# Optimization experiments

Hardware: AMD Instinct MI355X
Metric: run time of the kernel (lower is better)

## Reference

```python
import jax, jax.numpy as jnp
import numpy as np

D_MODEL, EMB_DIM, MLP_ORDER, SEQ_LEN, BATCH = 768, 3, 16, 8192, 8


def setup_inputs() -> dict:
    key = jax.random.key(0)
    ks = jax.random.split(key, 12)
    L = SEQ_LEN
    # PositionalEmbedding buffers (deterministic, as in __init__)
    t = jnp.linspace(0.0, 1.0, L)[None, :, None]                      # [1, L, 1]
    bands = (EMB_DIM - 1) // 2                                        # = 1
    t_long = jnp.linspace(0.0, L - 1.0, L)[None, :, None]
    w = 2.0 * jnp.pi * t_long / L
    f = jnp.linspace(1e-4, bands - 1.0, bands)[None, None]
    zc = jnp.exp(-1j * f * w)
    z = jnp.concatenate([t, zc.real, zc.imag], axis=-1).astype(jnp.float32)  # [1, L, 3]
    # ExponentialModulation deltas (deterministic)
    max_decay = jnp.log(0.01) / 0.3
    min_decay = jnp.log(0.01) / 1.5
    deltas = jnp.linspace(min_decay, max_decay, D_MODEL)[None, None].astype(jnp.float32)  # [1,1,D]
    s = 0.1
    return {
        "x": jax.random.normal(ks[0], (BATCH, D_MODEL, L), jnp.float32),
        "L": L,
        "z": z,
        "t": t.astype(jnp.float32),
        "deltas": deltas,
        "freq": jnp.ones((1, MLP_ORDER), jnp.float32),
        "W0": jax.random.normal(ks[1], (EMB_DIM, MLP_ORDER), jnp.float32) * s,
        "b0": jax.random.normal(ks[2], (MLP_ORDER,), jnp.float32) * s,
        "W1": jax.random.normal(ks[3], (MLP_ORDER, MLP_ORDER), jnp.float32) * s,
        "b1": jax.random.normal(ks[4], (MLP_ORDER,), jnp.float32) * s,
        "W2": jax.random.normal(ks[5], (MLP_ORDER, MLP_ORDER), jnp.float32) * s,
        "b2": jax.random.normal(ks[6], (MLP_ORDER,), jnp.float32) * s,
        "W3": jax.random.normal(ks[7], (MLP_ORDER, D_MODEL), jnp.float32) * s,
        "b3": jax.random.normal(ks[8], (D_MODEL,), jnp.float32) * s,
        "bias": jax.random.normal(ks[9], (D_MODEL,), jnp.float32),
    }


def reference(x, L, z, t, deltas, freq, W0, b0, W1, b1, W2, b2, W3, b3, bias):
    # filter generation: MLP with shared Sin activation, then exponential modulation
    zl = z[:, :L]
    h = jnp.sin(freq * (zl @ W0 + b0))
    h = jnp.sin(freq * (h @ W1 + b1))
    h = jnp.sin(freq * (h @ W2 + b2))
    h = h @ W3 + b3                               # [1, L, D]
    h = h * jnp.exp(-t[:, :L] * jnp.abs(deltas))  # exponential modulation
    k = h[0].T                                    # [D, L]
    # fftconv: causal long convolution via zero-padded FFT + skip x*bias
    fft_size = 2 * L
    y = jnp.fft.irfft(jnp.fft.rfft(x, n=fft_size) * jnp.fft.rfft(k, n=fft_size), n=fft_size)[..., :L]
    return y + x * bias[:, None]
```

## Files before the change

kernel.cpp:

```cpp
#include <hip/hip_runtime.h>
#include <math.h>


#define LSEQ 8192
#define NCH 768
#define NBATCH 8
#define NT 512

#define OFF_TWB  0
#define OFF_TW16 1024
#define OFF_TL   5124
#define OFF_TWC  6660
#define OFF_H    10240
#define OFF_KF   141312

__device__ __forceinline__ float2 cadd(float2 a, float2 b){ return make_float2(a.x+b.x, a.y+b.y); }
__device__ __forceinline__ float2 csub(float2 a, float2 b){ return make_float2(a.x-b.x, a.y-b.y); }
__device__ __forceinline__ float2 cmul(float2 a, float2 b){ return make_float2(a.x*b.x - a.y*b.y, a.x*b.y + a.y*b.x); }
__device__ __forceinline__ float2 mni(float2 a){ return make_float2(a.y, -a.x); }

__device__ __forceinline__ void wave_sync(){
    asm volatile("s_waitcnt lgkmcnt(0)" ::: "memory");
}

__device__ __forceinline__ int IDX(int i){ return i ^ (((i>>4) ^ (i>>8)) & 15); }
__device__ __forceinline__ int drev(int k){
    return ((k & 15) << 9) | (((k >> 4) & 15) << 5) | (((k >> 8) & 15) << 1) | (k >> 12);
}

#define C1 0.923879532511286756f
#define S1 0.382683432365089772f
#define R2 0.707106781186547524f

template<bool FULL>
__device__ __forceinline__ void dft16(float2 q[16]) {
    if constexpr (FULL) {
#pragma unroll
        for (int j = 0; j < 8; ++j) { float2 u=q[j], v=q[j+8]; q[j]=cadd(u,v); q[j+8]=csub(u,v); }
    }
    q[9]  = cmul(q[9],  make_float2( C1,-S1));
    q[10] = cmul(q[10], make_float2( R2,-R2));
    q[11] = cmul(q[11], make_float2( S1,-C1));
    q[12] = mni(q[12]);
    q[13] = cmul(q[13], make_float2(-S1,-C1));
    q[14] = cmul(q[14], make_float2(-R2,-R2));
    q[15] = cmul(q[15], make_float2(-C1,-S1));
#pragma unroll
    for (int b = 0; b < 16; b += 8) {
#pragma unroll
        for (int j = 0; j < 4; ++j) { float2 u=q[b+j], v=q[b+j+4]; q[b+j]=cadd(u,v); q[b+j+4]=csub(u,v); }
        q[b+5] = cmul(q[b+5], make_float2( R2,-R2));
        q[b+6] = mni(q[b+6]);
        q[b+7] = cmul(q[b+7], make_float2(-R2,-R2));
    }
#pragma unroll
    for (int b = 0; b < 16; b += 4) {
        float2 u0=q[b], v0=q[b+2], u1=q[b+1], v1=q[b+3];
        q[b]=cadd(u0,v0); q[b+2]=csub(u0,v0);
        q[b+1]=cadd(u1,v1); q[b+3]=mni(csub(u1,v1));
    }
#pragma unroll
    for (int b = 0; b < 16; b += 2) { float2 u=q[b], v=q[b+1]; q[b]=cadd(u,v); q[b+1]=csub(u,v); }
}

template<int PASS>
__device__ __forceinline__ int psb(int t) {
    if constexpr (PASS == 0) {
        return t ^ (((t>>4) ^ (t>>8)) & 15);
    } else if constexpr (PASS == 1) {
        int p = t & 31, hb = t >> 5;
        return ((hb<<9) | p) ^ (((p>>4) ^ (hb<<1)) & 15);
    } else {
        int h = t >> 1;
        return ((h<<5) | (t&1)) ^ (((h<<1) ^ (h>>3)) & 15);
    }
}
template<int PASS>
__device__ __forceinline__ int paddr(int sb, int r) {
    if constexpr (PASS == 0)      return (sb ^ (2*(r&7))) + (r<<9);
    else if constexpr (PASS == 1) return (sb ^ ((2*(r&7)) ^ (r>>3))) + (r<<5);
    else                          return sb ^ ((r<<1) ^ (r>>3));
}

template<int PASS, bool DIT, bool PRUNED>
__device__ __forceinline__ void r16p(float2* lds, const float2 (*twT)[68], int t) {
    static constexpr int RV[16] = {0,8,4,12,2,10,6,14,1,9,5,13,3,11,7,15};
    const int sb = psb<PASS>(t);
    int rL, rH = 0;
    if constexpr (PASS == 0) { rL = 32 + (t & 31); rH = (t >> 5) << 1; }
    else if constexpr (PASS == 1) { rL = t & 31; }
    else { rL = 64 + (t & 1); }
    float2 q[16];
    if constexpr (PRUNED) {
#pragma unroll
        for (int r = 0; r < 8; ++r) { q[r] = lds[paddr<PASS>(sb, r)]; q[r+8] = q[r]; }
    } else {
#pragma unroll
        for (int r = 0; r < 16; ++r) q[r] = lds[paddr<PASS>(sb, r)];
    }
    if constexpr (DIT) {
#pragma unroll
        for (int m = 1; m < 16; ++m) {
            float2 w = twT[m][rL];
            if constexpr (PASS == 0) w = cmul(w, twT[m][rH]);
            q[m] = cmul(q[m], w);
        }
        dft16<true>(q);
    } else {
        dft16<!PRUNED>(q);
#pragma unroll
        for (int m = 1; m < 16; ++m) {
            float2 w = twT[m][rL];
            if constexpr (PASS == 0) w = cmul(w, twT[m][rH]);
            q[RV[m]] = cmul(q[RV[m]], w);
        }
    }
#pragma unroll
    for (int m = 0; m < 16; ++m) lds[paddr<PASS>(sb, m)] = q[RV[m]];
}

__device__ __forceinline__ void load_twT(float2 (*twT)[68], const float* __restrict__ ws, int tid) {
    const float2* gTWB = (const float2*)(ws + OFF_TWB);
    const float2* gTL  = (const float2*)(ws + OFF_TL);
    const float2* gTWC = (const float2*)(ws + OFF_TWC);
    for (int idx = tid; idx < 16*66; idx += NT) {
        int r = idx >> 4, m = idx & 15;
        float2 v;
        if (r < 32)      v = gTWB[(r << 4) + m];
        else if (r < 64) v = gTL[((r - 32) << 4) + m];
        else             v = gTWC[((r - 64) << 4) + m];
        twT[m][r] = v;
    }
}

__device__ __forceinline__ void specpair(float2 V1, float2 V2, float4 kv, float2 W,
                                         float2& o1, float2& o2) {
    float2 Eh = make_float2(V1.x + V2.x, V1.y - V2.y);
    float2 Oh = make_float2(V1.y + V2.y, V2.x - V1.x);
    float2 S = make_float2(kv.x, kv.y);
    float a = W.x*kv.z, b = W.y*kv.w, cc = W.x*kv.w, dd = W.y*kv.z;
    float2 T  = make_float2(a - b, cc + dd);
    float2 T2 = make_float2(a + b, cc - dd);
    float2 Ep = cadd(cmul(Eh, S), cmul(Oh, T));
    float2 Op = cadd(cmul(Eh, T2), cmul(Oh, S));
    o1 = make_float2(Ep.y + Op.x, Ep.x - Op.y);
    o2 = make_float2(Op.x - Ep.y, Ep.x + Op.y);
}

__global__ __launch_bounds__(512) void k_pre(const float* __restrict__ z, const float* __restrict__ freq,
        const float* __restrict__ W0, const float* __restrict__ b0,
        const float* __restrict__ W1, const float* __restrict__ b1,
        const float* __restrict__ W2, const float* __restrict__ b2,
        float* __restrict__ ws, float* __restrict__ H) {
    __shared__ double2 lA[128], lB[128];
    const int t = threadIdx.x;
    if (blockIdx.x == 0) {
        const double K = -2.0 * 3.14159265358979323846 / 16384.0;
        if (t < 128)      { double a = K * (double)(t << 7); lA[t] = make_double2(cos(a), sin(a)); }
        else if (t < 256) { int b = t - 128; double a = K * (double)b; lB[b] = make_double2(cos(a), sin(a)); }
        __syncthreads();
        auto wf = [&](int e) -> float2 {
            e &= 16383;
            double2 A = lA[e >> 7], B = lB[e & 127];
            return make_float2((float)(A.x*B.x - A.y*B.y), (float)(A.x*B.y + A.y*B.x));
        };
        float2* tw16 = (float2*)(ws + OFF_TW16);
        for (int k = t; k <= 2048; k += 512) tw16[k] = wf(k);
        if (t < 32) {
            float2* rowL = (float2*)(ws + OFF_TL)  + (t << 4);
            float2* rowB = (float2*)(ws + OFF_TWB) + (t << 4);
#pragma unroll
            for (int m = 0; m < 16; ++m) { rowL[m] = wf(2*t*m); rowB[m] = wf(32*t*m); }
        } else if (t < 34) {
            int c2 = t - 32;
            float2* rowC = (float2*)(ws + OFF_TWC) + (c2 << 4);
#pragma unroll
            for (int m = 0; m < 16; ++m) rowC[m] = wf(512*c2*m);
        }
    } else {
        const int j = ((blockIdx.x - 1) << 9) + t;
        const float z0 = z[j*3+0], z1 = z[j*3+1], z2 = z[j*3+2];
        float h[16], g[16];
#pragma unroll
        for (int m = 0; m < 16; ++m)
            h[m] = sinf(freq[m] * (z0*W0[m] + z1*W0[16+m] + z2*W0[32+m] + b0[m]));
#pragma unroll
        for (int m = 0; m < 16; ++m) {
            float a = b1[m];
#pragma unroll
            for (int p = 0; p < 16; ++p) a += h[p] * W1[p*16+m];
            g[m] = sinf(freq[m] * a);
        }
#pragma unroll
        for (int m = 0; m < 16; ++m) {
            float a = b2[m];
#pragma unroll
            for (int p = 0; p < 16; ++p) a += g[p] * W2[p*16+m];
            h[m] = sinf(freq[m] * a);
        }
        float4* hp = (float4*)(H + (j << 4));
        hp[0] = make_float4(h[0],  h[1],  h[2],  h[3]);
        hp[1] = make_float4(h[4],  h[5],  h[6],  h[7]);
        hp[2] = make_float4(h[8],  h[9],  h[10], h[11]);
        hp[3] = make_float4(h[12], h[13], h[14], h[15]);
    }
}

__global__ __launch_bounds__(NT) void k_filter(const float* __restrict__ H, const float* __restrict__ t,
        const float* __restrict__ deltas, const float* __restrict__ W3,
        const float* __restrict__ b3, const float* __restrict__ ws,
        float* __restrict__ KfF) {
    __shared__ float2 lds[LSEQ];
    __shared__ float2 twT[16][68];
    const int c = blockIdx.x;
    const int tid = threadIdx.x;
    load_twT(twT, ws, tid);
    float4 w3a = make_float4(W3[0*NCH+c],  W3[1*NCH+c],  W3[2*NCH+c],  W3[3*NCH+c]);
    float4 w3b = make_float4(W3[4*NCH+c],  W3[5*NCH+c],  W3[6*NCH+c],  W3[7*NCH+c]);
    float4 w3c = make_float4(W3[8*NCH+c],  W3[9*NCH+c],  W3[10*NCH+c], W3[11*NCH+c]);
    float4 w3d = make_float4(W3[12*NCH+c], W3[13*NCH+c], W3[14*NCH+c], W3[15*NCH+c]);
    const float b3c = b3[c];
    const float ad = fabsf(deltas[c]);
    const int sbA = psb<0>(tid);
#pragma unroll 2
    for (int j = 0; j < 8; ++j) {
        int n = tid + (j << 9);
        const float4* hp = (const float4*)(H + (n << 5));
        float4 p0 = hp[0], p1 = hp[1], p2 = hp[2], p3 = hp[3];
        float4 q0 = hp[4], q1 = hp[5], q2 = hp[6], q3 = hp[7];
        float s0 = b3c + p0.x*w3a.x + p0.y*w3a.y + p0.z*w3a.z + p0.w*w3a.w
                       + p1.x*w3b.x + p1.y*w3b.y + p1.z*w3b.z + p1.w*w3b.w
                       + p2.x*w3c.x + p2.y*w3c.y + p2.z*w3c.z + p2.w*w3c.w
                       + p3.x*w3d.x + p3.y*w3d.y + p3.z*w3d.z + p3.w*w3d.w;
        float s1 = b3c + q0.x*w3a.x + q0.y*w3a.y + q0.z*w3a.z + q0.w*w3a.w
                       + q1.x*w3b.x + q1.y*w3b.y + q1.z*w3b.z + q1.w*w3b.w
                       + q2.x*w3c.x + q2.y*w3c.y + q2.z*w3c.z + q2.w*w3c.w
                       + q3.x*w3d.x + q3.y*w3d.y + q3.z*w3d.z + q3.w*w3d.w;
        float2 tv = ((const float2*)t)[n];
        lds[(sbA ^ (2*j)) + (j<<9)] = make_float2(s0 * expf(-tv.x*ad), s1 * expf(-tv.y*ad));
    }
    __syncthreads();
    r16p<0,false,true >(lds, twT, tid); __syncthreads();
    r16p<1,false,false>(lds, twT, tid); wave_sync();
    r16p<2,false,false>(lds, twT, tid); __syncthreads();

    float4* kf4 = (float4*)KfF + (size_t)c * 4096;
    const float2* tw16 = (const float2*)(ws + OFF_TW16);
    const float sc = 1.0f / 32768.0f;
#pragma unroll 2
    for (int it = 0; it < 4; ++it) {
        int k  = tid + 1 + (it << 9);
        int jj = 4096 - k;
        int pA = IDX(drev(k)), pB = IDX(drev(jj));
        float2 uA = lds[pA], vA = lds[pA^1];
        float2 uB = lds[pB], vB = lds[pB^1];
        float2 Vk = cadd(uA, vA), Vk4 = csub(uA, vA);
        float2 Vj = cadd(uB, vB), Vj4 = csub(uB, vB);
        float2 W  = tw16[k];
        float2 Wj = make_float2(-W.y, -W.x);
        {
            float2 E = make_float2(Vk.x + Vj4.x, Vk.y - Vj4.y);
            float2 O = make_float2(Vk.y + Vj4.y, Vj4.x - Vk.x);
            float2 D = cmul(W, O);
            kf4[k] = make_float4(E.x*sc, E.y*sc, D.x*sc, D.y*sc);
        }
        {
            float2 E = make_float2(Vj.x + Vk4.x, Vj.y - Vk4.y);
            float2 O = make_float2(Vj.y + Vk4.y, Vk4.x - Vj.x);
            float2 D = cmul(Wj, O);
            kf4[jj] = make_float4(E.x*sc, E.y*sc, D.x*sc, D.y*sc);
        }
    }
    if (tid == 0) {
        float2 u = lds[0], v = lds[1];
        float2 V0 = cadd(u, v), VN = csub(u, v);
        kf4[0] = make_float4((V0.x + V0.y)/16384.f, (V0.x - V0.y)/16384.f,
                             VN.x/8192.f, -VN.y/8192.f);
    }
}

__global__ __launch_bounds__(NT) void k_main(const float* __restrict__ x, const float* __restrict__ ws,
        const float* __restrict__ KfF, const float* __restrict__ bias,
        float* __restrict__ out) {
    __shared__ float2 lds[LSEQ];
    __shared__ float2 twT[16][68];
    const int bid = blockIdx.x;
    const int c = bid >> 1, half = bid & 1;
    const int tt = threadIdx.x;
    const float4* kf4 = (const float4*)KfF + (size_t)c * 4096;
    const float2* tw16 = (const float2*)(ws + OFF_TW16);
    const size_t rowstride = (size_t)NCH * LSEQ;
    const float* xbase = x + (size_t)(half*4) * rowstride + (size_t)c * LSEQ;
    float* obase = out + (size_t)(half*4) * rowstride + (size_t)c * LSEQ;
    const float bc = bias[c];

    const int EB = (tt << 1) ^ (((tt>>3) ^ (tt>>7)) & 15);

    load_twT(twT, ws, tt);

#pragma unroll 1
    for (int rr = 0; rr < 4; ++rr) {
        const float4* xr4 = (const float4*)(xbase + (size_t)rr * rowstride);
#pragma unroll
        for (int j = 0; j < 4; ++j) {
            float4 v = xr4[tt + (j<<9)];
            int a0 = (EB ^ (j<<2)) + (j<<10);
            lds[a0]   = make_float2(v.x, v.y);
            lds[a0^1] = make_float2(v.z, v.w);
        }
        __syncthreads();
        r16p<0,false,true >(lds, twT, tt); __syncthreads();
        r16p<1,false,false>(lds, twT, tt); wave_sync();
        r16p<2,false,false>(lds, twT, tt); __syncthreads();

#pragma unroll 1
        for (int it = 0; it < 4; ++it) {
            int k  = tt + 1 + (it << 9);
            int jj = 4096 - k;
            int pA = IDX(drev(k)), pB = IDX(drev(jj));
            float2 uA = lds[pA], vA = lds[pA^1];
            float2 uB = lds[pB], vB = lds[pB^1];
            float2 Vk = cadd(uA, vA), Vk4 = csub(uA, vA);
            float2 Vj = cadd(uB, vB), Vj4 = csub(uB, vB);
            float4 kvk = kf4[k], kvj = kf4[jj];
            float2 W  = tw16[k];
            float2 Wj = make_float2(-W.y, -W.x);
            float2 r1, r2, r1j, r2j;
            specpair(Vk, Vj4, kvk, W,  r1,  r2);
            specpair(Vj, Vk4, kvj, Wj, r1j, r2j);
            lds[pA]   = cadd(r1, r2j);  lds[pA^1] = csub(r1, r2j);
            lds[pB]   = cadd(r1j, r2);  lds[pB^1] = csub(r1j, r2);
        }
        if (tt == 0) {
            float2 u = lds[0], v = lds[1];
            float2 V0 = cadd(u, v), VN = csub(u, v);
            float4 kv = kf4[0];
            float U0 = V0.x + V0.y, UL = V0.x - V0.y;
            float re = U0*kv.x + UL*kv.y;
            float im = U0*kv.x - UL*kv.y;
            float2 s0 = make_float2(im, re);
            float2 P = make_float2(VN.x*kv.z + VN.y*kv.w, VN.x*kv.w - VN.y*kv.z);
            float2 s1 = make_float2(-P.y, P.x);
            lds[0] = cadd(s0, s1);
            lds[1] = csub(s0, s1);
        }
        __syncthreads();

        r16p<2,true,false>(lds, twT, tt); wave_sync();
        r16p<1,true,false>(lds, twT, tt); __syncthreads();
        r16p<0,true,false>(lds, twT, tt); __syncthreads();

        float4* orow4 = (float4*)(obase + (size_t)rr * rowstride);
#pragma unroll
        for (int j = 0; j < 4; ++j) {
            int a0 = (EB ^ (j<<2)) + (j<<10);
            float2 wA = lds[a0], wB = lds[a0^1];
            float4 xv = xr4[tt + (j<<9)];
            orow4[tt + (j<<9)] = make_float4(wA.y + xv.x*bc, wA.x + xv.y*bc,
                                             wB.y + xv.z*bc, wB.x + xv.w*bc);
        }
        if (rr < 3) __syncthreads();
    }
}

extern "C" void kernel_launch(void* const* d_in, const int* in_sizes, int n_in,
                              void* d_out, int out_size, void* d_ws, size_t ws_size,
                              hipStream_t stream) {
    const float* x      = (const float*)d_in[0];
    const float* z      = (const float*)d_in[2];
    const float* t      = (const float*)d_in[3];
    const float* deltas = (const float*)d_in[4];
    const float* freq   = (const float*)d_in[5];
    const float* W0     = (const float*)d_in[6];
    const float* b0     = (const float*)d_in[7];
    const float* W1     = (const float*)d_in[8];
    const float* b1     = (const float*)d_in[9];
    const float* W2     = (const float*)d_in[10];
    const float* b2     = (const float*)d_in[11];
    const float* W3     = (const float*)d_in[12];
    const float* b3     = (const float*)d_in[13];
    const float* bias   = (const float*)d_in[14];
    float* out = (float*)d_out;
    float* ws  = (float*)d_ws;
    float* H   = ws + OFF_H;
    float* Kf  = ws + OFF_KF;

    hipLaunchKernelGGL(k_pre, dim3(17), dim3(512), 0, stream, z, freq, W0, b0, W1, b1, W2, b2, ws, H);
    hipLaunchKernelGGL(k_filter, dim3(NCH), dim3(NT), 0, stream, H, t, deltas, W3, b3, ws, Kf);
    hipLaunchKernelGGL(k_main, dim3(NBATCH * NCH / 4), dim3(NT), 0, stream, x, ws, Kf, bias, out);
}
```

Measured before the change: 678.5 us.

## Process two FFT rows per block pass in main and filter kernels

The radix-16 FFT passes now transform two independent rows at once, using two LDS buffers and a shared twiddle load. k_main handles its four batch rows as two pairs, so it needs half as many barriers and gets more memory-level parallelism. k_filter computes two channels per block and launches half as many blocks. The cost is twice the LDS per block (about 136 KB) and higher register pressure, which lowers occupancy and may cause spills.

```diff
diff --git a/kernel.cpp b/kernel.cpp
--- a/kernel.cpp
+++ b/kernel.cpp
@@ -83,40 +83,49 @@
 }
 
 template<int PASS, bool DIT, bool PRUNED>
-__device__ __forceinline__ void r16p(float2* lds, const float2 (*twT)[68], int t) {
+__device__ __forceinline__ void r16p2(float2* l0, float2* l1, const float2 (*twT)[68], int t) {
     static constexpr int RV[16] = {0,8,4,12,2,10,6,14,1,9,5,13,3,11,7,15};
     const int sb = psb<PASS>(t);
     int rL, rH = 0;
     if constexpr (PASS == 0) { rL = 32 + (t & 31); rH = (t >> 5) << 1; }
     else if constexpr (PASS == 1) { rL = t & 31; }
     else { rL = 64 + (t & 1); }
-    float2 q[16];
+    float2 q0[16], q1[16];
     if constexpr (PRUNED) {
 #pragma unroll
-        for (int r = 0; r < 8; ++r) { q[r] = lds[paddr<PASS>(sb, r)]; q[r+8] = q[r]; }
+        for (int r = 0; r < 8; ++r) { q0[r] = l0[paddr<PASS>(sb, r)]; q1[r] = l1[paddr<PASS>(sb, r)]; }
+#pragma unroll
+        for (int r = 0; r < 8; ++r) { q0[r+8] = q0[r]; q1[r+8] = q1[r]; }
     } else {
 #pragma unroll
-        for (int r = 0; r < 16; ++r) q[r] = lds[paddr<PASS>(sb, r)];
+        for (int r = 0; r < 16; ++r) { q0[r] = l0[paddr<PASS>(sb, r)]; q1[r] = l1[paddr<PASS>(sb, r)]; }
     }
     if constexpr (DIT) {
 #pragma unroll
         for (int m = 1; m < 16; ++m) {
             float2 w = twT[m][rL];
             if constexpr (PASS == 0) w = cmul(w, twT[m][rH]);
-            q[m] = cmul(q[m], w);
-        }
-        dft16<true>(q);
+            q0[m] = cmul(q0[m], w);
+            q1[m] = cmul(q1[m], w);
+        }
+        dft16<true>(q0);
+        dft16<true>(q1);
     } else {
-        dft16<!PRUNED>(q);
+        dft16<!PRUNED>(q0);
+        dft16<!PRUNED>(q1);
 #pragma unroll
         for (int m = 1; m < 16; ++m) {
             float2 w = twT[m][rL];
             if constexpr (PASS == 0) w = cmul(w, twT[m][rH]);
-            q[RV[m]] = cmul(q[RV[m]], w);
-        }
-    }
-#pragma unroll
-    for (int m = 0; m < 16; ++m) lds[paddr<PASS>(sb, m)] = q[RV[m]];
+            q0[RV[m]] = cmul(q0[RV[m]], w);
+            q1[RV[m]] = cmul(q1[RV[m]], w);
+        }
+    }
+#pragma unroll
+    for (int m = 0; m < 16; ++m) {
+        l0[paddr<PASS>(sb, m)] = q0[RV[m]];
+        l1[paddr<PASS>(sb, m)] = q1[RV[m]];
+    }
 }
 
 __device__ __forceinline__ void load_twT(float2 (*twT)[68], const float* __restrict__ ws, int tid) {
@@ -145,6 +154,58 @@
     float2 Op = cadd(cmul(Eh, T2), cmul(Oh, S));
     o1 = make_float2(Ep.y + Op.x, Ep.x - Op.y);
     o2 = make_float2(Op.x - Ep.y, Ep.x + Op.y);
+}
+
+__device__ __forceinline__ void spec_rows(float2* l, int pA, int pB,
+                                          float4 kvk, float4 kvj, float2 W, float2 Wj) {
+    float2 uA = l[pA], vA = l[pA^1];
+    float2 uB = l[pB], vB = l[pB^1];
+    float2 Vk = cadd(uA, vA), Vk4 = csub(uA, vA);
+    float2 Vj = cadd(uB, vB), Vj4 = csub(uB, vB);
+    float2 r1, r2, r1j, r2j;
+    specpair(Vk, Vj4, kvk, W,  r1,  r2);
+    specpair(Vj, Vk4, kvj, Wj, r1j, r2j);
+    l[pA]   = cadd(r1, r2j);  l[pA^1] = csub(r1, r2j);
+    l[pB]   = cadd(r1j, r2);  l[pB^1] = csub(r1j, r2);
+}
+
+__device__ __forceinline__ void spec_dc(float2* l, float4 kv) {
+    float2 u = l[0], v = l[1];
+    float2 V0 = cadd(u, v), VN = csub(u, v);
+    float U0 = V0.x + V0.y, UL = V0.x - V0.y;
+    float re = U0*kv.x + UL*kv.y;
+    float im = U0*kv.x - UL*kv.y;
+    float2 s0 = make_float2(im, re);
+    float2 P = make_float2(VN.x*kv.z + VN.y*kv.w, VN.x*kv.w - VN.y*kv.z);
+    float2 s1 = make_float2(-P.y, P.x);
+    l[0] = cadd(s0, s1);
+    l[1] = csub(s0, s1);
+}
+
+__device__ __forceinline__ void filt_store(float2* l, float4* kf, int k, int jj,
+                                           int pA, int pB, float2 W, float2 Wj, float sc) {
+    float2 uA = l[pA], vA = l[pA^1];
+    float2 uB = l[pB], vB = l[pB^1];
+    float2 Vk = cadd(uA, vA), Vk4 = csub(uA, vA);
+    float2 Vj = cadd(uB, vB), Vj4 = csub(uB, vB);
+    {
+        float2 E = make_float2(Vk.x + Vj4.x, Vk.y - Vj4.y);
+        float2 O = make_float2(Vk.y + Vj4.y, Vj4.x - Vk.x);
+        float2 D = cmul(W, O);
+        kf[k] = make_float4(E.x*sc, E.y*sc, D.x*sc, D.y*sc);
+    }
+    {
+        float2 E = make_float2(Vj.x + Vk4.x, Vj.y - Vk4.y);
+        float2 O = make_float2(Vj.y + Vk4.y, Vk4.x - Vj.x);
+        float2 D = cmul(Wj, O);
+        kf[jj] = make_float4(E.x*sc, E.y*sc, D.x*sc, D.y*sc);
+    }
+}
+__device__ __forceinline__ void filt_dc(float2* l, float4* kf) {
+    float2 u = l[0], v = l[1];
+    float2 V0 = cadd(u, v), VN = csub(u, v);
+    kf[0] = make_float4((V0.x + V0.y)/16384.f, (V0.x - V0.y)/16384.f,
+                        VN.x/8192.f, -VN.y/8192.f);
 }
 
 __global__ __launch_bounds__(512) void k_pre(const float* __restrict__ z, const float* __restrict__ freq,
@@ -210,83 +271,70 @@
         const float* __restrict__ deltas, const float* __restrict__ W3,
         const float* __restrict__ b3, const float* __restrict__ ws,
         float* __restrict__ KfF) {
-    __shared__ float2 lds[LSEQ];
+    __shared__ float2 lds2[2][LSEQ];
     __shared__ float2 twT[16][68];
-    const int c = blockIdx.x;
+    const int c0 = blockIdx.x << 1, c1 = c0 + 1;
     const int tid = threadIdx.x;
+    float2* l0 = lds2[0];
+    float2* l1 = lds2[1];
     load_twT(twT, ws, tid);
-    float4 w3a = make_float4(W3[0*NCH+c],  W3[1*NCH+c],  W3[2*NCH+c],  W3[3*NCH+c]);
-    float4 w3b = make_float4(W3[4*NCH+c],  W3[5*NCH+c],  W3[6*NCH+c],  W3[7*NCH+c]);
-    float4 w3c = make_float4(W3[8*NCH+c],  W3[9*NCH+c],  W3[10*NCH+c], W3[11*NCH+c]);
-    float4 w3d = make_float4(W3[12*NCH+c], W3[13*NCH+c], W3[14*NCH+c], W3[15*NCH+c]);
-    const float b3c = b3[c];
-    const float ad = fabsf(deltas[c]);
+    float w30[16], w31[16];
+#pragma unroll
+    for (int m = 0; m < 16; ++m) { w30[m] = W3[m*NCH + c0]; w31[m] = W3[m*NCH + c1]; }
+    const float b30 = b3[c0], b31 = b3[c1];
+    const float ad0 = fabsf(deltas[c0]), ad1 = fabsf(deltas[c1]);
     const int sbA = psb<0>(tid);
-#pragma unroll 2
+#pragma unroll 1
     for (int j = 0; j < 8; ++j) {
         int n = tid + (j << 9);
         const float4* hp = (const float4*)(H + (n << 5));
-        float4 p0 = hp[0], p1 = hp[1], p2 = hp[2], p3 = hp[3];
-        float4 q0 = hp[4], q1 = hp[5], q2 = hp[6], q3 = hp[7];
-        float s0 = b3c + p0.x*w3a.x + p0.y*w3a.y + p0.z*w3a.z + p0.w*w3a.w
-                       + p1.x*w3b.x + p1.y*w3b.y + p1.z*w3b.z + p1.w*w3b.w
-                       + p2.x*w3c.x + p2.y*w3c.y + p2.z*w3c.z + p2.w*w3c.w
-                       + p3.x*w3d.x + p3.y*w3d.y + p3.z*w3d.z + p3.w*w3d.w;
-        float s1 = b3c + q0.x*w3a.x + q0.y*w3a.y + q0.z*w3a.z + q0.w*w3a.w
-                       + q1.x*w3b.x + q1.y*w3b.y + q1.z*w3b.z + q1.w*w3b.w
-                       + q2.x*w3c.x + q2.y*w3c.y + q2.z*w3c.z + q2.w*w3c.w
-                       + q3.x*w3d.x + q3.y*w3d.y + q3.z*w3d.z + q3.w*w3d.w;
+        float sA0 = b30, sB0 = b30, sA1 = b31, sB1 = b31;
+#pragma unroll
+        for (int q = 0; q < 4; ++q) {
+            float4 a = hp[q];
+            float4 b = hp[4+q];
+            sA0 += a.x*w30[4*q] + a.y*w30[4*q+1] + a.z*w30[4*q+2] + a.w*w30[4*q+3];
+            sB0 += b.x*w30[4*q] + b.y*w30[4*q+1] + b.z*w30[4*q+2] + b.w*w30[4*q+3];
+            sA1 += a.x*w31[4*q] + a.y*w31[4*q+1] + a.z*w31[4*q+2] + a.w*w31[4*q+3];
+            sB1 += b.x*w31[4*q] + b.y*w31[4*q+1] + b.z*w31[4*q+2] + b.w*w31[4*q+3];
+        }
         float2 tv = ((const float2*)t)[n];
-        lds[(sbA ^ (2*j)) + (j<<9)] = make_float2(s0 * expf(-tv.x*ad), s1 * expf(-tv.y*ad));
+        int a0 = (sbA ^ (2*j)) + (j<<9);
+        l0[a0] = make_float2(sA0 * expf(-tv.x*ad0), sB0 * expf(-tv.y*ad0));
+        l1[a0] = make_float2(sA1 * expf(-tv.x*ad1), sB1 * expf(-tv.y*ad1));
     }
     __syncthreads();
-    r16p<0,false,true >(lds, twT, tid); __syncthreads();
-    r16p<1,false,false>(lds, twT, tid); wave_sync();
-    r16p<2,false,false>(lds, twT, tid); __syncthreads();
-
-    float4* kf4 = (float4*)KfF + (size_t)c * 4096;
+    r16p2<0,false,true >(l0, l1, twT, tid); __syncthreads();
+    r16p2<1,false,false>(l0, l1, twT, tid); wave_sync();
+    r16p2<2,false,false>(l0, l1, twT, tid); __syncthreads();
+
+    float4* kf0 = (float4*)KfF + (size_t)c0 * 4096;
+    float4* kf1 = (float4*)KfF + (size_t)c1 * 4096;
     const float2* tw16 = (const float2*)(ws + OFF_TW16);
     const float sc = 1.0f / 32768.0f;
-#pragma unroll 2
+#pragma unroll 1
     for (int it = 0; it < 4; ++it) {
         int k  = tid + 1 + (it << 9);
         int jj = 4096 - k;
         int pA = IDX(drev(k)), pB = IDX(drev(jj));
-        float2 uA = lds[pA], vA = lds[pA^1];
-        float2 uB = lds[pB], vB = lds[pB^1];
-        float2 Vk = cadd(uA, vA), Vk4 = csub(uA, vA);
-        float2 Vj = cadd(uB, vB), Vj4 = csub(uB, vB);
         float2 W  = tw16[k];
         float2 Wj = make_float2(-W.y, -W.x);
-        {
-            float2 E = make_float2(Vk.x + Vj4.x, Vk.y - Vj4.y);
-            float2 O = make_float2(Vk.y + Vj4.y, Vj4.x - Vk.x);
-            float2 D = cmul(W, O);
-            kf4[k] = make_float4(E.x*sc, E.y*sc, D.x*sc, D.y*sc);
-        }
-        {
-            float2 E = make_float2(Vj.x + Vk4.x, Vj.y - Vk4.y);
-            float2 O = make_float2(Vj.y + Vk4.y, Vk4.x - Vj.x);
-            float2 D = cmul(Wj, O);
-            kf4[jj] = make_float4(E.x*sc, E.y*sc, D.x*sc, D.y*sc);
-        }
-    }
-    if (tid == 0) {
-        float2 u = lds[0], v = lds[1];
-        float2 V0 = cadd(u, v), VN = csub(u, v);
-        kf4[0] = make_float4((V0.x + V0.y)/16384.f, (V0.x - V0.y)/16384.f,
-                             VN.x/8192.f, -VN.y/8192.f);
-    }
+        filt_store(l0, kf0, k, jj, pA, pB, W, Wj, sc);
+        filt_store(l1, kf1, k, jj, pA, pB, W, Wj, sc);
+    }
+    if (tid == 0) { filt_dc(l0, kf0); filt_dc(l1, kf1); }
 }
 
 __global__ __launch_bounds__(NT) void k_main(const float* __restrict__ x, const float* __restrict__ ws,
         const float* __restrict__ KfF, const float* __restrict__ bias,
         float* __restrict__ out) {
-    __shared__ float2 lds[LSEQ];
+    __shared__ float2 lds2[2][LSEQ];
     __shared__ float2 twT[16][68];
     const int bid = blockIdx.x;
     const int c = bid >> 1, half = bid & 1;
     const int tt = threadIdx.x;
+    float2* l0 = lds2[0];
+    float2* l1 = lds2[1];
     const float4* kf4 = (const float4*)KfF + (size_t)c * 4096;
     const float2* tw16 = (const float2*)(ws + OFF_TW16);
     const size_t rowstride = (size_t)NCH * LSEQ;
@@ -299,67 +347,61 @@
     load_twT(twT, ws, tt);
 
 #pragma unroll 1
-    for (int rr = 0; rr < 4; ++rr) {
-        const float4* xr4 = (const float4*)(xbase + (size_t)rr * rowstride);
+    for (int pp = 0; pp < 2; ++pp) {
+        const float4* xr0 = (const float4*)(xbase + (size_t)(2*pp)     * rowstride);
+        const float4* xr1 = (const float4*)(xbase + (size_t)(2*pp + 1) * rowstride);
 #pragma unroll
         for (int j = 0; j < 4; ++j) {
-            float4 v = xr4[tt + (j<<9)];
+            float4 v0 = xr0[tt + (j<<9)];
+            float4 v1 = xr1[tt + (j<<9)];
             int a0 = (EB ^ (j<<2)) + (j<<10);
-            lds[a0]   = make_float2(v.x, v.y);
-            lds[a0^1] = make_float2(v.z, v.w);
+            l0[a0]   = make_float2(v0.x, v0.y);
+            l0[a0^1] = make_float2(v0.z, v0.w);
+            l1[a0]   = make_float2(v1.x, v1.y);
+            l1[a0^1] = make_float2(v1.z, v1.w);
         }
         __syncthreads();
-        r16p<0,false,true >(lds, twT, tt); __syncthreads();
-        r16p<1,false,false>(lds, twT, tt); wave_sync();
-        r16p<2,false,false>(lds, twT, tt); __syncthreads();
+        r16p2<0,false,true >(l0, l1, twT, tt); __syncthreads();
+        r16p2<1,false,false>(l0, l1, twT, tt); wave_sync();
+        r16p2<2,false,false>(l0, l1, twT, tt); __syncthreads();
 
 #pragma unroll 1
         for (int it = 0; it < 4; ++it) {
             int k  = tt + 1 + (it << 9);
             int jj = 4096 - k;
             int pA = IDX(drev(k)), pB = IDX(drev(jj));
-            float2 uA = lds[pA], vA = lds[pA^1];
-            float2 uB = lds[pB], vB = lds[pB^1];
-            float2 Vk = cadd(uA, vA), Vk4 = csub(uA, vA);
-            float2 Vj = cadd(uB, vB), Vj4 = csub(uB, vB);
             float4 kvk = kf4[k], kvj = kf4[jj];
             float2 W  = tw16[k];
             float2 Wj = make_float2(-W.y, -W.x);
-            float2 r1, r2, r1j, r2j;
-            specpair(Vk, Vj4, kvk, W,  r1,  r2);
-            specpair(Vj, Vk4, kvj, Wj, r1j, r2j);
-            lds[pA]   = cadd(r1, r2j);  lds[pA^1] = csub(r1, r2j);
-            lds[pB]   = cadd(r1j, r2);  lds[pB^1] = csub(r1j, r2);
+            spec_rows(l0, pA, pB, kvk, kvj, W, Wj);
+            spec_rows(l1, pA, pB, kvk, kvj, W, Wj);
         }
         if (tt == 0) {
-            float2 u = lds[0], v = lds[1];
-            float2 V0 = cadd(u, v), VN = csub(u, v);
             float4 kv = kf4[0];
-            float U0 = V0.x + V0.y, UL = V0.x - V0.y;
-            float re = U0*kv.x + UL*kv.y;
-            float im = U0*kv.x - UL*kv.y;
-            float2 s0 = make_float2(im, re);
-            float2 P = make_float2(VN.x*kv.z + VN.y*kv.w, VN.x*kv.w - VN.y*kv.z);
-            float2 s1 = make_float2(-P.y, P.x);
-            lds[0] = cadd(s0, s1);
-            lds[1] = csub(s0, s1);
+            spec_dc(l0, kv);
+            spec_dc(l1, kv);
         }
         __syncthreads();
 
-        r16p<2,true,false>(lds, twT, tt); wave_sync();
-        r16p<1,true,false>(lds, twT, tt); __syncthreads();
-        r16p<0,true,false>(lds, twT, tt); __syncthreads();
-
-        float4* orow4 = (float4*)(obase + (size_t)rr * rowstride);
+        r16p2<2,true,false>(l0, l1, twT, tt); wave_sync();
+        r16p2<1,true,false>(l0, l1, twT, tt); __syncthreads();
+        r16p2<0,true,false>(l0, l1, twT, tt); __syncthreads();
+
+        float4* o0 = (float4*)(obase + (size_t)(2*pp)     * rowstride);
+        float4* o1 = (float4*)(obase + (size_t)(2*pp + 1) * rowstride);
 #pragma unroll
         for (int j = 0; j < 4; ++j) {
             int a0 = (EB ^ (j<<2)) + (j<<10);
-            float2 wA = lds[a0], wB = lds[a0^1];
-            float4 xv = xr4[tt + (j<<9)];
-            orow4[tt + (j<<9)] = make_float4(wA.y + xv.x*bc, wA.x + xv.y*bc,
-                                             wB.y + xv.z*bc, wB.x + xv.w*bc);
-        }
-        if (rr < 3) __syncthreads();
+            float2 wA0 = l0[a0], wB0 = l0[a0^1];
+            float2 wA1 = l1[a0], wB1 = l1[a0^1];
+            float4 xv0 = xr0[tt + (j<<9)];
+            float4 xv1 = xr1[tt + (j<<9)];
+            o0[tt + (j<<9)] = make_float4(wA0.y + xv0.x*bc, wA0.x + xv0.y*bc,
+                                          wB0.y + xv0.z*bc, wB0.x + xv0.w*bc);
+            o1[tt + (j<<9)] = make_float4(wA1.y + xv1.x*bc, wA1.x + xv1.y*bc,
+                                          wB1.y + xv1.z*bc, wB1.x + xv1.w*bc);
+        }
+        if (pp == 0) __syncthreads();
     }
 }
 
@@ -386,6 +428,6 @@
     float* Kf  = ws + OFF_KF;
 
     hipLaunchKernelGGL(k_pre, dim3(17), dim3(512), 0, stream, z, freq, W0, b0, W1, b1, W2, b2, ws, H);
-    hipLaunchKernelGGL(k_filter, dim3(NCH), dim3(NT), 0, stream, H, t, deltas, W3, b3, ws, Kf);
+    hipLaunchKernelGGL(k_filter, dim3(NCH/2), dim3(NT), 0, stream, H, t, deltas, W3, b3, ws, Kf);
     hipLaunchKernelGGL(k_main, dim3(NBATCH * NCH / 4), dim3(NT), 0, stream, x, ws, Kf, bias, out);
 }
```

Result: no change. 672.0 us (-1.0%).
